# Performance work log

Measured on AMD Instinct MI355X. Metric: run time of the kernel, lower is better.

## Reference

```python
import jax, jax.numpy as jnp
import numpy as np

TEMPERATURE = 0.07
NORMALIZE = True
NEG_INF = -1e30


def setup_inputs() -> dict:
    key = jax.random.key(0)
    features = jax.random.normal(key, (8192, 512), dtype=jnp.float32)
    return {"features": features}


def reference(features):
    # features: [B, D]
    B = features.shape[0]
    if NORMALIZE:
        norm = jnp.linalg.norm(features, axis=1, keepdims=True)
        features = features / jnp.maximum(norm, 1e-12)
    # [B, B] similarity matrix
    sim = jnp.matmul(features, features.T) / TEMPERATURE

    # default SimCLR labels: arange(B//2) repeated twice -> pair (i, i + B//2)
    half = jnp.arange(B // 2, dtype=jnp.int32)
    labels = jnp.concatenate([half, half])
    eq = labels[None, :] == labels[:, None]          # [B, B]
    diag = jnp.eye(B, dtype=bool)
    mask_pos = eq & ~diag                            # positives per row

    # Original per-row CE: logits = cat(pos_sims, neg_sims) (= all j != i),
    # target index 0 = FIRST positive (lowest column index). Loss_i =
    # logsumexp_{j != i}(sim[i, j]) - sim[i, first_pos_i].
    sim_masked = jnp.where(diag, NEG_INF, sim)
    lse = jax.scipy.special.logsumexp(sim_masked, axis=1)   # [B]

    first_pos = jnp.argmax(mask_pos, axis=1)                 # first True per row
    pos_sim = jnp.take_along_axis(sim, first_pos[:, None], axis=1)[:, 0]

    has_pos = jnp.any(mask_pos, axis=1)
    losses = jnp.where(has_pos, lse - pos_sim, 0.0)
    count = jnp.maximum(jnp.sum(has_pos.astype(jnp.float32)), 1.0)
    return jnp.sum(losses) / count
```

## Files before the change

kernel.cpp:

```cpp
#include <hip/hip_runtime.h>
#include <hip/hip_bf16.h>
#include <stdint.h>

#define BATCH 8192
#define DIM   512
#define TILE  128
#define BK    64
#define NT    (BATCH / TILE)
#define NPAIR (NT * (NT + 1) / 2)

#define FEAT_SCALE 4.5398164f
#define LN2        0.69314718055994531f

typedef __attribute__((ext_vector_type(8))) short short8;
typedef __attribute__((ext_vector_type(4))) float f32x4;

__device__ __forceinline__ void gld_lds16(const void* g, void* l) {
  __builtin_amdgcn_global_load_lds(
      (__attribute__((address_space(1))) void*)(uintptr_t)g,
      (__attribute__((address_space(3))) void*)(uintptr_t)l,
      16, 0, 0);
}

__global__ __launch_bounds__(256) void normalize_bf16(
    const float* __restrict__ x, __hip_bfloat16* __restrict__ o,
    float* __restrict__ rowsum) {
  const int wv = threadIdx.x >> 6, lane = threadIdx.x & 63;
  const int row = blockIdx.x * 4 + wv;
  if (lane == 0) rowsum[row] = 0.0f;
  const float4* xr = (const float4*)(x + (size_t)row * DIM);
  const float4 v0 = xr[lane];
  const float4 v1 = xr[lane + 64];
  float ss = v0.x * v0.x + v0.y * v0.y + v0.z * v0.z + v0.w * v0.w +
             v1.x * v1.x + v1.y * v1.y + v1.z * v1.z + v1.w * v1.w;
#pragma unroll
  for (int m = 32; m > 0; m >>= 1) ss += __shfl_xor(ss, m, 64);
  const float inv = FEAT_SCALE / fmaxf(sqrtf(ss), 1e-12f);
  ushort4 p0, p1;
  p0.x = __bfloat16_as_ushort(__float2bfloat16(v0.x * inv));
  p0.y = __bfloat16_as_ushort(__float2bfloat16(v0.y * inv));
  p0.z = __bfloat16_as_ushort(__float2bfloat16(v0.z * inv));
  p0.w = __bfloat16_as_ushort(__float2bfloat16(v0.w * inv));
  p1.x = __bfloat16_as_ushort(__float2bfloat16(v1.x * inv));
  p1.y = __bfloat16_as_ushort(__float2bfloat16(v1.y * inv));
  p1.z = __bfloat16_as_ushort(__float2bfloat16(v1.z * inv));
  p1.w = __bfloat16_as_ushort(__float2bfloat16(v1.w * inv));
  ushort4* orow = (ushort4*)(o + (size_t)row * DIM);
  orow[lane]      = p0;
  orow[lane + 64] = p1;
}

__global__ __launch_bounds__(256, 4) void sim_lse_kernel(
    const __hip_bfloat16* __restrict__ F, float* __restrict__ rowsum,
    float* __restrict__ possim) {
  __shared__ __hip_bfloat16 smem[2 * TILE * BK];
  __shared__ float colAcc[TILE];

  const int t = blockIdx.x;
  int by = (int)((129.0f - sqrtf(129.0f * 129.0f - 8.0f * (float)t)) * 0.5f);
  if (by > NT - 1) by = NT - 1;
  if (by < 0) by = 0;
  while ((by + 1) * (129 - (by + 1)) / 2 <= t) ++by;
  while (by * (129 - by) / 2 > t) --by;
  const int bx = by + (t - by * (129 - by) / 2);
  const bool diagTile = (bx == by);

  const int rowBase = by * TILE;
  const int colBase = bx * TILE;

  const int tid   = threadIdx.x;
  const int lane  = tid & 63;
  const int wv    = tid >> 6;
  const int waveM = wv >> 1;
  const int waveN = wv & 1;
  const int quad  = lane >> 4;
  const int l15   = lane & 15;

  if (tid < TILE) colAcc[tid] = 0.0f;

  f32x4 acc[4][4] = {};

  const int sb = lane & 7;
  const __hip_bfloat16* gA[4];
  const __hip_bfloat16* gB[4];
  char* ldsA[4];
  char* ldsB[4];
#pragma unroll
  for (int c = 0; c < 4; ++c) {
    const int sRow = wv * 32 + c * 8 + (lane >> 3);
    const int g = sb ^ (sRow & 7);
    gA[c] = F + (size_t)(rowBase + sRow) * DIM + g * 8;
    gB[c] = F + (size_t)(colBase + sRow) * DIM + g * 8;
    ldsA[c] = (char*)smem + (wv * 4 + c) * 1024;
    ldsB[c] = (char*)smem + 16384 + (wv * 4 + c) * 1024;
  }

  int aOff[4], bOff[4];
#pragma unroll
  for (int i = 0; i < 4; ++i) {
    const int Ra = waveM * 64 + i * 16 + l15;
    aOff[i] = Ra * 128 + (quad ^ (Ra & 7)) * 16;
    const int Rb = waveN * 64 + i * 16 + l15;
    bOff[i] = 16384 + Rb * 128 + (quad ^ (Rb & 7)) * 16;
  }
  char* sbase = (char*)smem;

  for (int k0 = 0; k0 < DIM; k0 += BK) {
#pragma unroll
    for (int c = 0; c < 4; ++c) {
      gld_lds16(gA[c] + k0, ldsA[c]);
      gld_lds16(gB[c] + k0, ldsB[c]);
    }
    __syncthreads();

    short8 a[4], b[4];
#pragma unroll
    for (int i = 0; i < 4; ++i) {
      a[i] = *(const short8*)(sbase + aOff[i]);
      b[i] = *(const short8*)(sbase + bOff[i]);
    }
#pragma unroll
    for (int mi = 0; mi < 4; ++mi)
#pragma unroll
      for (int ni = 0; ni < 4; ++ni)
        acc[mi][ni] =
            __builtin_amdgcn_mfma_f32_16x16x32_bf16(a[mi], b[ni], acc[mi][ni], 0, 0, 0);
#pragma unroll
    for (int i = 0; i < 4; ++i) {
      a[i] = *(const short8*)(sbase + (aOff[i] ^ 64));
      b[i] = *(const short8*)(sbase + (bOff[i] ^ 64));
    }
#pragma unroll
    for (int mi = 0; mi < 4; ++mi)
#pragma unroll
      for (int ni = 0; ni < 4; ++ni)
        acc[mi][ni] =
            __builtin_amdgcn_mfma_f32_16x16x32_bf16(a[mi], b[ni], acc[mi][ni], 0, 0, 0);
    __syncthreads();
  }

  float* redBuf = (float*)smem;
  f32x4 rsumv[4] = {};
  float colpart[4] = {0.0f, 0.0f, 0.0f, 0.0f};

  if (diagTile) {
#pragma unroll
    for (int mi = 0; mi < 4; ++mi)
#pragma unroll
      for (int ni = 0; ni < 4; ++ni)
#pragma unroll
        for (int r = 0; r < 4; ++r) {
          const int rl = waveM * 64 + mi * 16 + quad * 4 + r;
          const int cl = waveN * 64 + ni * 16 + l15;
          rsumv[mi][r] += (cl == rl) ? 0.0f : exp2f(acc[mi][ni][r]);
        }
  } else {
    const bool hasPos = (bx == by + 32);
#pragma unroll
    for (int mi = 0; mi < 4; ++mi)
#pragma unroll
      for (int ni = 0; ni < 4; ++ni)
#pragma unroll
        for (int r = 0; r < 4; ++r) {
          const float s = acc[mi][ni][r];
          const float e = exp2f(s);
          rsumv[mi][r] += e;
          colpart[ni] += e;
          if (hasPos) {
            const int rl = waveM * 64 + mi * 16 + quad * 4 + r;
            const int cl = waveN * 64 + ni * 16 + l15;
            if (cl == rl) {
              const int gi = rowBase + rl;
              possim[gi] = s;
              possim[gi + 4096] = s;
            }
          }
        }
  }

  {
    float* wbase = redBuf + ((waveN * 2 + waveM) * 16 + l15) * 68 + quad * 4;
#pragma unroll
    for (int mi = 0; mi < 4; ++mi)
      *(f32x4*)(wbase + mi * 16) = rsumv[mi];
  }

  if (!diagTile) {
#pragma unroll
    for (int ni = 0; ni < 4; ++ni) {
      float c = colpart[ni];
      c += __shfl_xor(c, 16, 64);
      c += __shfl_xor(c, 32, 64);
      if (quad == 0) atomicAdd(&colAcc[waveN * 64 + ni * 16 + l15], c);
    }
  }
  __syncthreads();

  {
    const int wn = tid >> 7, r = tid & 127;
    const int strip = r >> 6, rl = r & 63;
    const float* base = redBuf + ((wn * 2 + strip) * 16) * 68 + rl;
    float s = 0.0f;
#pragma unroll
    for (int j = 0; j < 16; ++j) s += base[j * 68];
    atomicAdd(&rowsum[rowBase + r], s);
  }
  if (tid < TILE && !diagTile)
    atomicAdd(&rowsum[colBase + tid], colAcc[tid]);
}

__global__ __launch_bounds__(1024) void finalize_kernel(
    const float* __restrict__ rowsum, const float* __restrict__ possim,
    float* __restrict__ out) {
  float acc = 0.0f;
  for (int i = threadIdx.x; i < BATCH; i += 1024)
    acc += __logf(rowsum[i]) - possim[i] * LN2;
#pragma unroll
  for (int m = 32; m > 0; m >>= 1) acc += __shfl_xor(acc, m, 64);
  __shared__ float ws[16];
  const int lane = threadIdx.x & 63, wv = threadIdx.x >> 6;
  if (lane == 0) ws[wv] = acc;
  __syncthreads();
  if (threadIdx.x == 0) {
    float tot = 0.0f;
#pragma unroll
    for (int k = 0; k < 16; ++k) tot += ws[k];
    out[0] = tot * (1.0f / (float)BATCH);
  }
}

extern "C" void kernel_launch(void* const* d_in, const int* in_sizes, int n_in,
                              void* d_out, int out_size, void* d_ws, size_t ws_size,
                              hipStream_t stream) {
  const float* x = (const float*)d_in[0];
  float* out = (float*)d_out;

  __hip_bfloat16* Fb = (__hip_bfloat16*)d_ws;
  float* rowsum = (float*)((char*)d_ws + (size_t)BATCH * DIM * sizeof(__hip_bfloat16));
  float* possim = rowsum + BATCH;

  normalize_bf16<<<BATCH / 4, 256, 0, stream>>>(x, Fb, rowsum);
  sim_lse_kernel<<<NPAIR, 256, 0, stream>>>(Fb, rowsum, possim);
  finalize_kernel<<<1, 1024, 0, stream>>>(rowsum, possim, out);
}
```

Baseline: 111.7 us.

## Double-buffer LDS k-loop with BK=32 and fuse finalize via last-block counter

The GEMM k-loop now uses BK=32 with two LDS buffers, prefetching the next k-slice via global_load_lds while MFMAs consume the current one, instead of load-sync-compute-sync per step. The separate finalize kernel is removed: each block bumps a global counter after its atomics, and the last block computes the log-sum reduction and writes the output, saving one launch. The risks are a missing sync between the prefetch and the reads, and the extra fence/atomic per block.

```diff
diff --git a/kernel.cpp b/kernel.cpp
--- a/kernel.cpp
+++ b/kernel.cpp
@@ -5,7 +5,8 @@
 #define BATCH 8192
 #define DIM   512
 #define TILE  128
-#define BK    64
+#define BK    32
+#define NITER (DIM / BK)
 #define NT    (BATCH / TILE)
 #define NPAIR (NT * (NT + 1) / 2)
 
@@ -24,10 +25,11 @@
 
 __global__ __launch_bounds__(256) void normalize_bf16(
     const float* __restrict__ x, __hip_bfloat16* __restrict__ o,
-    float* __restrict__ rowsum) {
+    float* __restrict__ rowsum, int* __restrict__ doneCount) {
   const int wv = threadIdx.x >> 6, lane = threadIdx.x & 63;
   const int row = blockIdx.x * 4 + wv;
   if (lane == 0) rowsum[row] = 0.0f;
+  if (blockIdx.x == 0 && threadIdx.x == 0) *doneCount = 0;
   const float4* xr = (const float4*)(x + (size_t)row * DIM);
   const float4 v0 = xr[lane];
   const float4 v1 = xr[lane + 64];
@@ -52,9 +54,11 @@
 
 __global__ __launch_bounds__(256, 4) void sim_lse_kernel(
     const __hip_bfloat16* __restrict__ F, float* __restrict__ rowsum,
-    float* __restrict__ possim) {
-  __shared__ __hip_bfloat16 smem[2 * TILE * BK];
+    float* __restrict__ possim, int* __restrict__ doneCount,
+    float* __restrict__ out) {
+  __shared__ __hip_bfloat16 smem[2 * TILE * BK * 2];
   __shared__ float colAcc[TILE];
+  __shared__ int lastFlag;
 
   const int t = blockIdx.x;
   int by = (int)((129.0f - sqrtf(129.0f * 129.0f - 8.0f * (float)t)) * 0.5f);
@@ -80,55 +84,55 @@
 
   f32x4 acc[4][4] = {};
 
-  const int sb = lane & 7;
-  const __hip_bfloat16* gA[4];
-  const __hip_bfloat16* gB[4];
-  char* ldsA[4];
-  char* ldsB[4];
-#pragma unroll
-  for (int c = 0; c < 4; ++c) {
-    const int sRow = wv * 32 + c * 8 + (lane >> 3);
-    const int g = sb ^ (sRow & 7);
+  const int sb   = lane & 3;
+  const int r16  = lane >> 2;
+  const __hip_bfloat16* gA[2];
+  const __hip_bfloat16* gB[2];
+  int ldsAoff[2], ldsBoff[2];
+#pragma unroll
+  for (int c = 0; c < 2; ++c) {
+    const int sRow = wv * 32 + c * 16 + r16;
+    const int g = sb ^ ((sRow >> 1) & 3);
     gA[c] = F + (size_t)(rowBase + sRow) * DIM + g * 8;
     gB[c] = F + (size_t)(colBase + sRow) * DIM + g * 8;
-    ldsA[c] = (char*)smem + (wv * 4 + c) * 1024;
-    ldsB[c] = (char*)smem + 16384 + (wv * 4 + c) * 1024;
+    ldsAoff[c] = (wv * 2 + c) * 1024;
+    ldsBoff[c] = 8192 + (wv * 2 + c) * 1024;
   }
 
   int aOff[4], bOff[4];
 #pragma unroll
   for (int i = 0; i < 4; ++i) {
     const int Ra = waveM * 64 + i * 16 + l15;
-    aOff[i] = Ra * 128 + (quad ^ (Ra & 7)) * 16;
+    aOff[i] = Ra * 64 + (quad ^ ((Ra >> 1) & 3)) * 16;
     const int Rb = waveN * 64 + i * 16 + l15;
-    bOff[i] = 16384 + Rb * 128 + (quad ^ (Rb & 7)) * 16;
+    bOff[i] = 8192 + Rb * 64 + (quad ^ ((Rb >> 1) & 3)) * 16;
   }
   char* sbase = (char*)smem;
 
-  for (int k0 = 0; k0 < DIM; k0 += BK) {
-#pragma unroll
-    for (int c = 0; c < 4; ++c) {
-      gld_lds16(gA[c] + k0, ldsA[c]);
-      gld_lds16(gB[c] + k0, ldsB[c]);
+#pragma unroll
+  for (int c = 0; c < 2; ++c) {
+    gld_lds16(gA[c], sbase + ldsAoff[c]);
+    gld_lds16(gB[c], sbase + ldsBoff[c]);
+  }
+  __syncthreads();
+
+#pragma unroll
+  for (int it = 0; it < NITER; ++it) {
+    const int cur = (it & 1) * 16384;
+    const int nxt = ((it + 1) & 1) * 16384;
+    if (it + 1 < NITER) {
+      const int k0 = (it + 1) * BK;
+#pragma unroll
+      for (int c = 0; c < 2; ++c) {
+        gld_lds16(gA[c] + k0, sbase + nxt + ldsAoff[c]);
+        gld_lds16(gB[c] + k0, sbase + nxt + ldsBoff[c]);
+      }
     }
-    __syncthreads();
-
     short8 a[4], b[4];
 #pragma unroll
     for (int i = 0; i < 4; ++i) {
-      a[i] = *(const short8*)(sbase + aOff[i]);
-      b[i] = *(const short8*)(sbase + bOff[i]);
-    }
-#pragma unroll
-    for (int mi = 0; mi < 4; ++mi)
-#pragma unroll
-      for (int ni = 0; ni < 4; ++ni)
-        acc[mi][ni] =
-            __builtin_amdgcn_mfma_f32_16x16x32_bf16(a[mi], b[ni], acc[mi][ni], 0, 0, 0);
-#pragma unroll
-    for (int i = 0; i < 4; ++i) {
-      a[i] = *(const short8*)(sbase + (aOff[i] ^ 64));
-      b[i] = *(const short8*)(sbase + (bOff[i] ^ 64));
+      a[i] = *(const short8*)(sbase + cur + aOff[i]);
+      b[i] = *(const short8*)(sbase + cur + bOff[i]);
     }
 #pragma unroll
     for (int mi = 0; mi < 4; ++mi)
@@ -207,25 +211,28 @@
   }
   if (tid < TILE && !diagTile)
     atomicAdd(&rowsum[colBase + tid], colAcc[tid]);
-}
-
-__global__ __launch_bounds__(1024) void finalize_kernel(
-    const float* __restrict__ rowsum, const float* __restrict__ possim,
-    float* __restrict__ out) {
-  float acc = 0.0f;
-  for (int i = threadIdx.x; i < BATCH; i += 1024)
-    acc += __logf(rowsum[i]) - possim[i] * LN2;
-#pragma unroll
-  for (int m = 32; m > 0; m >>= 1) acc += __shfl_xor(acc, m, 64);
-  __shared__ float ws[16];
-  const int lane = threadIdx.x & 63, wv = threadIdx.x >> 6;
-  if (lane == 0) ws[wv] = acc;
-  __syncthreads();
-  if (threadIdx.x == 0) {
-    float tot = 0.0f;
-#pragma unroll
-    for (int k = 0; k < 16; ++k) tot += ws[k];
-    out[0] = tot * (1.0f / (float)BATCH);
+
+  __syncthreads();
+  if (tid == 0) {
+    __threadfence();
+    const int prev = atomicAdd(doneCount, 1);
+    lastFlag = (prev == NPAIR - 1) ? 1 : 0;
+  }
+  __syncthreads();
+  if (lastFlag) {
+    __threadfence();
+    volatile const float* rs = rowsum;
+    volatile const float* ps = possim;
+    float acc2 = 0.0f;
+    for (int i = tid; i < BATCH; i += 256)
+      acc2 += __logf(rs[i]) - ps[i] * LN2;
+#pragma unroll
+    for (int m = 32; m > 0; m >>= 1) acc2 += __shfl_xor(acc2, m, 64);
+    if (lane == 0) redBuf[wv] = acc2;
+    __syncthreads();
+    if (tid == 0)
+      out[0] = (redBuf[0] + redBuf[1] + redBuf[2] + redBuf[3]) *
+               (1.0f / (float)BATCH);
   }
 }
 
@@ -238,8 +245,8 @@
   __hip_bfloat16* Fb = (__hip_bfloat16*)d_ws;
   float* rowsum = (float*)((char*)d_ws + (size_t)BATCH * DIM * sizeof(__hip_bfloat16));
   float* possim = rowsum + BATCH;
-
-  normalize_bf16<<<BATCH / 4, 256, 0, stream>>>(x, Fb, rowsum);
-  sim_lse_kernel<<<NPAIR, 256, 0, stream>>>(Fb, rowsum, possim);
-  finalize_kernel<<<1, 1024, 0, stream>>>(rowsum, possim, out);
-}
+  int* doneCount = (int*)(possim + BATCH);
+
+  normalize_bf16<<<BATCH / 4, 256, 0, stream>>>(x, Fb, rowsum, doneCount);
+  sim_lse_kernel<<<NPAIR, 256, 0, stream>>>(Fb, rowsum, possim, doneCount, out);
+}
```

Result: slower. 172.0 us (+54.0%).
